# Performance work log

Hardware: AMD Instinct MI355X
Metric: run time of the kernel (lower is better)

## Reference

```python
import jax, jax.numpy as jnp
import numpy as np
import math

EPS = 1e-5

def make_coords(H, W):
    # Faithful port of generate_coordinates (batch-independent; channels 8,9 stay zero).
    cy = H / 2.0 - 0.5
    cx = W / 2.0 - 0.5
    gx, gy = np.meshgrid(np.arange(H, dtype=np.float32), np.arange(W, dtype=np.float32), indexing='ij')
    two_pi = 2.0 * math.pi
    theta = np.arctan2(gy - cx, gx - cy) % two_pi
    theta = np.round(10000.0 * theta) / 10000.0
    coords = np.zeros((H, W, 18), dtype=np.float32)
    adds = [(1, 1), (1, 0), (1, -1), (0, 1), None, (0, -1), (-1, 1), (-1, 0), (-1, -1)]
    for k, add in enumerate(adds):
        if add is None:
            continue  # center tap offset left at zero (as in source)
        n = k if k < 4 else k - 1
        a = theta + n * (two_pi / 8.0)
        coords[:, :, 2 * k] = np.cos(a) + add[0]
        coords[:, :, 2 * k + 1] = np.sin(a) + add[1]
    return jnp.asarray(coords)

def bilinear_sample(x, py, px):
    # x: [B,C,H,W]; py/px: [H,W] sample coords; zero outside boundaries (torchvision semantics).
    H, W = x.shape[2], x.shape[3]
    y0f = jnp.floor(py); x0f = jnp.floor(px)
    wy1 = py - y0f; wy0 = 1.0 - wy1
    wx1 = px - x0f; wx0 = 1.0 - wx1
    def gather(yf, xf):
        valid = ((yf >= 0) & (yf < H) & (xf >= 0) & (xf < W)).astype(x.dtype)
        yi = jnp.clip(yf, 0, H - 1).astype(jnp.int32)
        xi = jnp.clip(xf, 0, W - 1).astype(jnp.int32)
        return x[:, :, yi, xi] * valid  # [B,C,H,W]
    return (gather(y0f, x0f) * (wy0 * wx0) + gather(y0f, x0f + 1) * (wy0 * wx1)
            + gather(y0f + 1, x0f) * (wy1 * wx0) + gather(y0f + 1, x0f + 1) * (wy1 * wx1))

def deform_conv(x, coords, weight, pad=1):
    # x: [B,Cin,H,W]; coords: [H,W,18] with (dy,dx) pairs per 3x3 tap; weight: [Cout,Cin,3,3]; no bias.
    B, C, H, W = x.shape
    ys = jnp.arange(H, dtype=x.dtype)[:, None]
    xs = jnp.arange(W, dtype=x.dtype)[None, :]
    out = jnp.zeros((B, weight.shape[0], H, W), x.dtype)
    for k in range(9):  # fixed 3x3 taps
        kh, kw = k // 3, k % 3
        py = ys - pad + kh + coords[..., 2 * k]
        px = xs - pad + kw + coords[..., 2 * k + 1]
        samp = bilinear_sample(x, py, px)
        out = out + jnp.einsum('bchw,oc->bohw', samp, weight[:, :, kh, kw])
    return out

def bn_relu(x, gamma, beta):
    # BatchNorm2d in training mode (batch statistics, biased variance) + ReLU.
    mu = x.mean(axis=(0, 2, 3), keepdims=True)
    var = ((x - mu) ** 2).mean(axis=(0, 2, 3), keepdims=True)
    xn = (x - mu) * jax.lax.rsqrt(var + EPS)
    return jax.nn.relu(xn * gamma[None, :, None, None] + beta[None, :, None, None])

def maxpool2(x):
    B, C, H, W = x.shape
    return x.reshape(B, C, H // 2, 2, W // 2, 2).max(axis=(3, 5))

def setup_inputs() -> dict:
    key = jax.random.key(0)
    ks = jax.random.split(key, 16)
    B = 1024
    def conv_w(k, co, ci):
        return jax.random.normal(k, (co, ci, 3, 3), jnp.float32) * (1.0 / np.sqrt(ci * 9))
    inp = {
        'x': jax.random.normal(ks[0], (B, 1, 32, 32), jnp.float32),
        'w11': conv_w(ks[1], 32, 1),  'g11': jnp.ones(32),  'b11': jnp.zeros(32),
        'w12': conv_w(ks[2], 32, 32), 'g12': jnp.ones(32),  'b12': jnp.zeros(32),
        'w21': conv_w(ks[3], 64, 32), 'g21': jnp.ones(64),  'b21': jnp.zeros(64),
        'w22': conv_w(ks[4], 64, 64), 'g22': jnp.ones(64),  'b22': jnp.zeros(64),
        'w31': conv_w(ks[5], 128, 64),  'g31': jnp.ones(128), 'b31': jnp.zeros(128),
        'w32': conv_w(ks[6], 128, 128), 'g32': jnp.ones(128), 'b32': jnp.zeros(128),
        'fcw': jax.random.normal(ks[7], (10, 128), jnp.float32) * (1.0 / np.sqrt(128)),
        'fcb': jnp.zeros(10),
        'c32': make_coords(32, 32),
        'c16': make_coords(16, 16),
        'c8': make_coords(8, 8),
    }
    return inp

def reference(x, w11, g11, b11, w12, g12, b12, w21, g21, b21, w22, g22, b22,
              w31, g31, b31, w32, g32, b32, fcw, fcb, c32, c16, c8):
    x = bn_relu(deform_conv(x, c32, w11), g11, b11)
    x = bn_relu(deform_conv(x, c32, w12), g12, b12)
    x = maxpool2(x)                      # [B,32,16,16]
    x = bn_relu(deform_conv(x, c16, w21), g21, b21)
    x = bn_relu(deform_conv(x, c16, w22), g22, b22)
    x = maxpool2(x)                      # [B,64,8,8]
    x = bn_relu(deform_conv(x, c8, w31), g31, b31)
    x = bn_relu(deform_conv(x, c8, w32), g32, b32)
    x = x.mean(axis=(2, 3))              # AvgPool2d(8) over full 8x8 -> [B,128]
    return x @ fcw.T + fcb               # [B,10]
```

## Files before the change

kernel.cpp:

```cpp
#include <hip/hip_runtime.h>
#include <math.h>


#define BATCH 1024
typedef unsigned short u16;
typedef unsigned int uint;
typedef _Float16 f16;
typedef __attribute__((ext_vector_type(2))) _Float16 f16x2;
typedef __attribute__((ext_vector_type(8))) _Float16 f16x8;
typedef __attribute__((ext_vector_type(4))) float f32x4;

__device__ __forceinline__ float b2f(u16 v) {
    return __uint_as_float(((uint)v) << 16);
}
__device__ __forceinline__ float ldf(const void* p, long long i, int isbf) {
    return isbf ? b2f(((const u16*)p)[i]) : ((const float*)p)[i];
}
__device__ __forceinline__ f16x2 u2h2(uint u) {
    union { uint u; f16x2 h; } c; c.u = u; return c.h;
}
__device__ __forceinline__ uint h22u(f16x2 h) {
    union { uint u; f16x2 h; } c; c.h = h; return c.u;
}
__device__ __forceinline__ float h2f(u16 v) {
    union { u16 u; f16 h; } c; c.u = v; return (float)c.h;
}
__device__ __forceinline__ u16 f2h(float f) {
    union { u16 u; f16 h; } c; c.h = (f16)f; return c.u;
}
__device__ __forceinline__ f16x2 pkh(float a, float b) {
    union { decltype(__builtin_amdgcn_cvt_pkrtz(0.f, 0.f)) v; f16x2 h; } c;
    c.v = __builtin_amdgcn_cvt_pkrtz(a, b);
    return c.h;
}

struct Ptrs { const void* p[24]; int sz[24]; };

__global__ __launch_bounds__(256) void probe_dtype(Ptrs P, int* __restrict__ flags)
{
    int t = blockIdx.x;
    bool ones = (t == 2 || t == 5 || t == 8 || t == 11 || t == 14 || t == 17);
    bool inh  = (t == 3 || t == 6 || t == 9 || t == 12 || t == 15 || t == 18 || t == 20);
    if (inh) return;
    const u16* q = (const u16*)P.p[t];
    if (ones) {
        if (threadIdx.x == 0) {
            uint w0 = *(const uint*)q;
            flags[t] = (w0 == 0x3F803F80u) ? 1 : 0;
        }
        return;
    }
    int n = P.sz[t]; if (n > 4096) n = 4096;
    __shared__ int cnt;
    if (threadIdx.x == 0) cnt = 0;
    __syncthreads();
    int local = 0;
    for (int i = threadIdx.x; i < n; i += 256) {
        uint e = (q[i] >> 7) & 0xFFu;
        if (!(e == 0u || (e >= 100u && e <= 140u))) local++;
    }
    atomicAdd(&cnt, local);
    __syncthreads();
    if (threadIdx.x == 0) flags[t] = (cnt * 8 > n) ? 0 : 1;
}

__global__ void fixup_flags(int* __restrict__ flags)
{
    if (threadIdx.x == 0) {
        flags[3] = flags[2];  flags[6] = flags[5];  flags[9] = flags[8];
        flags[12] = flags[11]; flags[15] = flags[14]; flags[18] = flags[17];
        flags[20] = flags[19];
    }
}

__device__ void table_body(const void* coords, int H, int W,
                           int* tIdx, float* tW, int fcd, int i)
{
    int HW = H * W;
    if (i >= HW * 9) return;
    int p = i / 9, k = i % 9;
    int h = p / W, w = p % W;
    int kh = k / 3, kw = k % 3;
    float py = (float)(h - 1 + kh) + ldf(coords, p * 18 + 2 * k, fcd);
    float px = (float)(w - 1 + kw) + ldf(coords, p * 18 + 2 * k + 1, fcd);
    float y0f = floorf(py), x0f = floorf(px);
    float wy1 = py - y0f, wy0 = 1.0f - wy1;
    float wx1 = px - x0f, wx0 = 1.0f - wx1;
    int y0 = (int)y0f, x0 = (int)x0f;
#pragma unroll
    for (int j = 0; j < 4; ++j) {
        int dy = j >> 1, dx = j & 1;
        int yy = y0 + dy, xx = x0 + dx;
        bool valid = (yy >= 0) && (yy < H) && (xx >= 0) && (xx < W);
        int yc = min(max(yy, 0), H - 1);
        int xc = min(max(xx, 0), W - 1);
        tIdx[i * 4 + j] = yc * W + xc;
        tW[i * 4 + j] = valid ? (dy ? wy1 : wy0) * (dx ? wx1 : wx0) : 0.0f;
    }
}

__global__ __launch_bounds__(256) void build_tables(
    const void* c32, const void* c16, const void* c8,
    int* tI32, float* tW32, int* tI16, float* tW16, int* tI8, float* tW8,
    const int* __restrict__ flags)
{
    int b = blockIdx.x, t = threadIdx.x;
    if (b < 36)      table_body(c32, 32, 32, tI32, tW32, flags[21], b * 256 + t);
    else if (b < 45) table_body(c16, 16, 16, tI16, tW16, flags[22], (b - 36) * 256 + t);
    else             table_body(c8, 8, 8, tI8, tW8, flags[23], (b - 45) * 256 + t);
}

__global__ __launch_bounds__(256) void transpose_in(
    const void* __restrict__ x, u16* __restrict__ X0, const int* __restrict__ flags)
{
    int fx = flags[0];
    int p = blockIdx.x;
    int t = threadIdx.x;
    ushort4 v;
    v.x = f2h(ldf(x, (long long)(4 * t + 0) * 1024 + p, fx));
    v.y = f2h(ldf(x, (long long)(4 * t + 1) * 1024 + p, fx));
    v.z = f2h(ldf(x, (long long)(4 * t + 2) * 1024 + p, fx));
    v.w = f2h(ldf(x, (long long)(4 * t + 3) * 1024 + p, fx));
    ((ushort4*)(X0 + (size_t)p * BATCH))[t] = v;
}

__device__ void wb_body(const void* W, u16* Wb, int Cout, int Cin, int fw, int i)
{
    int c8 = i & 7;
    int r = i >> 3;
    int m = r % Cout;
    int r2 = r / Cout;
    int noct = Cin >> 3;
    int oc = r2 % noct;
    int k = r2 / noct;
    int c = oc * 8 + c8;
    Wb[i] = f2h(ldf(W, (long long)m * Cin * 9 + c * 9 + k, fw));
}

__global__ __launch_bounds__(256) void prep_all(
    const void* w11, const void* w12, const void* w21, const void* w22,
    const void* w31, const void* w32,
    float* w11p, u16* wb12, u16* wb21, u16* wb22, u16* wb31, u16* wb32,
    const int* __restrict__ flags)
{
    int i = blockIdx.x * 256 + threadIdx.x;
    if (i < 288) {
        int o = i / 9, k = i % 9;
        w11p[k * 32 + o] = ldf(w11, i, flags[1]);
    } else if (i < 9504)   wb_body(w12, wb12, 32, 32, flags[4], i - 288);
    else if (i < 27936)    wb_body(w21, wb21, 64, 32, flags[7], i - 9504);
    else if (i < 64800)    wb_body(w22, wb22, 64, 64, flags[10], i - 27936);
    else if (i < 138528)   wb_body(w31, wb31, 128, 64, flags[13], i - 64800);
    else if (i < 285984)   wb_body(w32, wb32, 128, 128, flags[16], i - 138528);
}

__global__ __launch_bounds__(256) void conv_l11(
    const u16* __restrict__ X0, const float* __restrict__ W2,
    u16* __restrict__ Y, const int* __restrict__ tIdx, const float* __restrict__ tW)
{
    const int id = blockIdx.x;
    const int p = id >> 1;
    const int oBase = (id & 1) * 16;
    const int b4 = threadIdx.x;
    const ushort4* Xu = (const ushort4*)X0;

    float4 acc[16];
#pragma unroll
    for (int o = 0; o < 16; ++o) acc[o] = make_float4(0.f, 0.f, 0.f, 0.f);

#pragma unroll
    for (int k = 0; k < 9; ++k) {
        float4 s = make_float4(0.f, 0.f, 0.f, 0.f);
#pragma unroll
        for (int j = 0; j < 4; ++j) {
            float wgt = tW[p * 36 + k * 4 + j];
            int pix = tIdx[p * 36 + k * 4 + j];
            ushort4 vv = Xu[pix * 256 + b4];
            s.x = fmaf(wgt, h2f(vv.x), s.x); s.y = fmaf(wgt, h2f(vv.y), s.y);
            s.z = fmaf(wgt, h2f(vv.z), s.z); s.w = fmaf(wgt, h2f(vv.w), s.w);
        }
#pragma unroll
        for (int o = 0; o < 16; ++o) {
            float wv = W2[k * 32 + oBase + o];
            acc[o].x = fmaf(wv, s.x, acc[o].x); acc[o].y = fmaf(wv, s.y, acc[o].y);
            acc[o].z = fmaf(wv, s.z, acc[o].z); acc[o].w = fmaf(wv, s.w, acc[o].w);
        }
    }
#pragma unroll
    for (int bb = 0; bb < 4; ++bb) {
        u16 h[16];
#pragma unroll
        for (int o = 0; o < 16; ++o) h[o] = f2h((&acc[o].x)[bb]);
        uint4 pk;
        pk.x = (uint)h[0] | ((uint)h[1] << 16);
        pk.y = (uint)h[2] | ((uint)h[3] << 16);
        pk.z = (uint)h[4] | ((uint)h[5] << 16);
        pk.w = (uint)h[6] | ((uint)h[7] << 16);
        uint4 pk2;
        pk2.x = (uint)h[8] | ((uint)h[9] << 16);
        pk2.y = (uint)h[10] | ((uint)h[11] << 16);
        pk2.z = (uint)h[12] | ((uint)h[13] << 16);
        pk2.w = (uint)h[14] | ((uint)h[15] << 16);
        size_t base = ((size_t)p * 1024 + 4 * b4 + bb) * 32 + oBase;
        *(uint4*)(Y + base) = pk;
        *(uint4*)(Y + base + 8) = pk2;
    }
}

template<int MF, int NF, int BNORM>
__global__ __launch_bounds__(256) void conv_mfma(
    const u16* __restrict__ X, const u16* __restrict__ Wb,
    u16* __restrict__ Y,
    const int* __restrict__ tIdx, const float* __restrict__ tW,
    int Cin, int Cout, int HW, int pshift,
    const float* __restrict__ stats, const void* __restrict__ gamma,
    const void* __restrict__ beta, const int* __restrict__ flags,
    int gslot, int bslot, float invN)
{
    __shared__ float sSC[128], sSH[128];
    if (BNORM) {
        if (threadIdx.x < Cin) {
            int c = threadIdx.x;
            float mean = stats[2 * c] * invN;
            float var = stats[2 * c + 1] * invN - mean * mean;
            float sc = ldf(gamma, c, flags[gslot]) * rsqrtf(var + 1e-5f);
            sSC[c] = sc;
            sSH[c] = ldf(beta, c, flags[bslot]) - mean * sc;
        }
        __syncthreads();
    }

    const int tid = threadIdx.x;
    const int wid = tid >> 6;
    const int lane = tid & 63;
    const int quad = lane >> 4;
    const int l16 = lane & 15;

    const int pper = HW >> 3;
    const int xcd = blockIdx.x & 7;
    const int lid = blockIdx.x >> 3;
    const int p = xcd * pper + (lid & (pper - 1));
    const int yq = lid >> pshift;

    const int nb = yq * (4 * NF * 16);
    const int wn = wid * (NF * 16);

    const int noct = Cin >> 3;
    const size_t pixstride = (size_t)1024 * Cin;

    int roff[NF];
#pragma unroll
    for (int nf = 0; nf < NF; ++nf)
        roff[nf] = (nb + wn + nf * 16 + l16) * Cin + quad * 8;

    f32x4 acc[MF][NF];
#pragma unroll
    for (int mf = 0; mf < MF; ++mf)
#pragma unroll
        for (int nf = 0; nf < NF; ++nf)
            acc[mf][nf] = (f32x4){0.f, 0.f, 0.f, 0.f};

    const f16x2 zeroh = (f16x2){(f16)0, (f16)0};
    const int nc = Cin >> 5;
    for (int cc = 0; cc < nc; ++cc) {
        const int coff = cc << 5;
        f16x2 sc2[4], sh2[4];
        if (BNORM) {
            int c0 = coff + quad * 8;
#pragma unroll
            for (int i = 0; i < 4; ++i) {
                sc2[i] = pkh(sSC[c0 + 2 * i], sSC[c0 + 2 * i + 1]);
                sh2[i] = pkh(sSH[c0 + 2 * i], sSH[c0 + 2 * i + 1]);
            }
        }
        for (int k = 0; k < 9; ++k) {
            int pix[4]; f16x2 wwh[4];
#pragma unroll
            for (int j = 0; j < 4; ++j) {
                pix[j] = __builtin_amdgcn_readfirstlane(tIdx[p * 36 + k * 4 + j]);
                float w = __uint_as_float(__builtin_amdgcn_readfirstlane(
                    __float_as_uint(tW[p * 36 + k * 4 + j])));
                wwh[j] = pkh(w, w);
            }
            const u16* xb0 = X + (size_t)pix[0] * pixstride;
            const u16* xb1 = X + (size_t)pix[1] * pixstride;
            const u16* xb2 = X + (size_t)pix[2] * pixstride;
            const u16* xb3 = X + (size_t)pix[3] * pixstride;

            f16x8 bf[NF];
#pragma unroll
            for (int nf = 0; nf < NF; ++nf) {
                int ro = roff[nf] + coff;
                uint4 v0 = *(const uint4*)(xb0 + ro);
                uint4 v1 = *(const uint4*)(xb1 + ro);
                uint4 v2 = *(const uint4*)(xb2 + ro);
                uint4 v3 = *(const uint4*)(xb3 + ro);
                const uint* a0 = &v0.x; const uint* a1 = &v1.x;
                const uint* a2 = &v2.x; const uint* a3 = &v3.x;
                union { f16x8 h; uint4 u; } cvt;
                uint o[4];
#pragma unroll
                for (int i = 0; i < 4; ++i) {
                    f16x2 t0 = u2h2(a0[i]), t1 = u2h2(a1[i]);
                    f16x2 t2 = u2h2(a2[i]), t3 = u2h2(a3[i]);
                    if (BNORM) {
                        t0 = __builtin_elementwise_max(t0 * sc2[i] + sh2[i], zeroh);
                        t1 = __builtin_elementwise_max(t1 * sc2[i] + sh2[i], zeroh);
                        t2 = __builtin_elementwise_max(t2 * sc2[i] + sh2[i], zeroh);
                        t3 = __builtin_elementwise_max(t3 * sc2[i] + sh2[i], zeroh);
                    }
                    f16x2 a = t0 * wwh[0];
                    a = t1 * wwh[1] + a;
                    a = t2 * wwh[2] + a;
                    a = t3 * wwh[3] + a;
                    o[i] = h22u(a);
                }
                cvt.u.x = o[0]; cvt.u.y = o[1]; cvt.u.z = o[2]; cvt.u.w = o[3];
                bf[nf] = cvt.h;
            }
            const u16* wk = Wb + ((size_t)(k * noct + (cc << 2) + quad) * Cout + l16) * 8;
#pragma unroll
            for (int mf = 0; mf < MF; ++mf) {
                const f16x8 af = *(const f16x8*)(wk + (size_t)mf * 16 * 8);
#pragma unroll
                for (int nf = 0; nf < NF; ++nf)
                    acc[mf][nf] = __builtin_amdgcn_mfma_f32_16x16x32_f16(
                        af, bf[nf], acc[mf][nf], 0, 0, 0);
            }
        }
    }

#pragma unroll
    for (int mf = 0; mf < MF; ++mf) {
        int cout0 = mf * 16 + quad * 4;
#pragma unroll
        for (int nf = 0; nf < NF; ++nf) {
            int b = nb + wn + nf * 16 + l16;
            uint2 pk;
            pk.x = h22u(pkh(acc[mf][nf][0], acc[mf][nf][1]));
            pk.y = h22u(pkh(acc[mf][nf][2], acc[mf][nf][3]));
            *(uint2*)(Y + ((size_t)p * 1024 + b) * Cout + cout0) = pk;
        }
    }
}

__global__ __launch_bounds__(256) void bn_stats2(
    const u16* __restrict__ Y, float* __restrict__ stats, int Cin, long long NPB)
{
    const int stride = Cin >> 3;
    const int RPI = 256 / stride;
    const int t = threadIdx.x;
    const int cg = t % stride;
    const int r = t / stride;
    const int lane = t & 63;
    const int wid = t >> 6;

    float s[8], q[8];
#pragma unroll
    for (int j = 0; j < 8; ++j) { s[j] = 0.f; q[j] = 0.f; }

    for (long long row0 = (long long)blockIdx.x * RPI; row0 < NPB;
         row0 += (long long)gridDim.x * RPI) {
        long long row = row0 + r;
        if (row >= NPB) continue;
        uint4 v = *(const uint4*)(Y + row * Cin + cg * 8);
        uint ua[4] = {v.x, v.y, v.z, v.w};
#pragma unroll
        for (int jj = 0; jj < 4; ++jj) {
            f16x2 h = u2h2(ua[jj]);
            float lo = (float)h.x, hi = (float)h.y;
            s[2 * jj] += lo;     q[2 * jj] += lo * lo;
            s[2 * jj + 1] += hi; q[2 * jj + 1] += hi * hi;
        }
    }
    for (int off = 32; off >= stride; off >>= 1) {
#pragma unroll
        for (int j = 0; j < 8; ++j) {
            s[j] += __shfl_down(s[j], off);
            q[j] += __shfl_down(q[j], off);
        }
    }
    __shared__ float rs[4][128], rq[4][128];
    if (lane < stride) {
#pragma unroll
        for (int j = 0; j < 8; ++j) {
            rs[wid][lane * 8 + j] = s[j];
            rq[wid][lane * 8 + j] = q[j];
        }
    }
    __syncthreads();
    if (t < Cin) {
        float S = rs[0][t] + rs[1][t] + rs[2][t] + rs[3][t];
        float Q = rq[0][t] + rq[1][t] + rq[2][t] + rq[3][t];
        atomicAdd(&stats[2 * t], S);
        atomicAdd(&stats[2 * t + 1], Q);
    }
}

__global__ __launch_bounds__(256) void pool_bn(
    const u16* __restrict__ A, u16* __restrict__ P,
    const float* __restrict__ stats,
    const void* __restrict__ gamma, const void* __restrict__ beta,
    const int* __restrict__ flags, int gslot, int bslot,
    int H2, int W2, int C, float invN, long long total)
{
    __shared__ float sSC[128], sSH[128];
    if (threadIdx.x < C) {
        int c = threadIdx.x;
        float mean = stats[2 * c] * invN;
        float var = stats[2 * c + 1] * invN - mean * mean;
        float sc = ldf(gamma, c, flags[gslot]) * rsqrtf(var + 1e-5f);
        sSC[c] = sc;
        sSH[c] = ldf(beta, c, flags[bslot]) - mean * sc;
    }
    __syncthreads();
    long long i = (long long)blockIdx.x * 256 + threadIdx.x;
    if (i >= total) return;
    int cgn = C >> 3;
    int cg = (int)(i % cgn);
    long long row = i / cgn;
    int b = (int)(row & 1023);
    int p2 = (int)(row >> 10);
    int h2 = p2 / W2, w2 = p2 % W2;
    int W = 2 * W2;
    int p00 = (2 * h2) * W + 2 * w2;
    const u16* base = A + (size_t)cg * 8;
    uint4 va = *(const uint4*)(base + ((size_t)(p00)*1024 + b) * C);
    uint4 vb = *(const uint4*)(base + ((size_t)(p00 + 1) * 1024 + b) * C);
    uint4 vd = *(const uint4*)(base + ((size_t)(p00 + W) * 1024 + b) * C);
    uint4 ve = *(const uint4*)(base + ((size_t)(p00 + W + 1) * 1024 + b) * C);
    uint ra[4] = {va.x, va.y, va.z, va.w};
    uint rb[4] = {vb.x, vb.y, vb.z, vb.w};
    uint rd[4] = {vd.x, vd.y, vd.z, vd.w};
    uint re[4] = {ve.x, ve.y, ve.z, ve.w};
    uint ro[4];
#pragma unroll
    for (int j = 0; j < 4; ++j) {
        int c = cg * 8 + 2 * j;
        f16x2 ha = u2h2(ra[j]), hb = u2h2(rb[j]), hd = u2h2(rd[j]), he = u2h2(re[j]);
        f16x2 hm = __builtin_elementwise_max(
            __builtin_elementwise_max(ha, hb), __builtin_elementwise_max(hd, he));
        float lo = fmaxf(fmaf((float)hm.x, sSC[c], sSH[c]), 0.f);
        float hi = fmaxf(fmaf((float)hm.y, sSC[c + 1], sSH[c + 1]), 0.f);
        ro[j] = h22u(pkh(lo, hi));
    }
    uint4 m; m.x = ro[0]; m.y = ro[1]; m.z = ro[2]; m.w = ro[3];
    *(uint4*)(P + ((size_t)p2 * 1024 + b) * C + cg * 8) = m;
}

__global__ __launch_bounds__(256) void avg_bn(
    const u16* __restrict__ A, float* __restrict__ M,
    const float* __restrict__ stats,
    const void* __restrict__ gamma, const void* __restrict__ beta,
    const int* __restrict__ flags, int gslot, int bslot, float invN)
{
    __shared__ float sSC[128], sSH[128];
    if (threadIdx.x < 128) {
        int c = threadIdx.x;
        float mean = stats[2 * c] * invN;
        float var = stats[2 * c + 1] * invN - mean * mean;
        float sc = ldf(gamma, c, flags[gslot]) * rsqrtf(var + 1e-5f);
        sSC[c] = sc;
        sSH[c] = ldf(beta, c, flags[bslot]) - mean * sc;
    }
    __syncthreads();
    int i = blockIdx.x * 256 + threadIdx.x;
    int b = i >> 4, cg = i & 15;
    float s[8];
#pragma unroll
    for (int j = 0; j < 8; ++j) s[j] = 0.f;
    for (int p = 0; p < 64; ++p) {
        uint4 v = *(const uint4*)(A + ((size_t)p * 1024 + b) * 128 + cg * 8);
        uint ua[4] = {v.x, v.y, v.z, v.w};
#pragma unroll
        for (int jj = 0; jj < 4; ++jj) {
            int c = cg * 8 + 2 * jj;
            f16x2 h = u2h2(ua[jj]);
            s[2 * jj] += fmaxf(fmaf((float)h.x, sSC[c], sSH[c]), 0.f);
            s[2 * jj + 1] += fmaxf(fmaf((float)h.y, sSC[c + 1], sSH[c + 1]), 0.f);
        }
    }
#pragma unroll
    for (int j = 0; j < 8; ++j) M[(size_t)b * 128 + cg * 8 + j] = s[j] * (1.0f / 64.0f);
}

__global__ __launch_bounds__(256) void fc_naive(
    const float* __restrict__ M, const void* __restrict__ fcw,
    const void* __restrict__ fcb, float* __restrict__ out, int total,
    const int* __restrict__ flags)
{
    int fw = flags[19], fb = flags[20];
    int i = blockIdx.x * 256 + threadIdx.x;
    if (i >= total) return;
    int o = i % 10, b = i / 10;
    float acc = ldf(fcb, o, fb);
    const float* Mb = M + (size_t)b * 128;
    for (int c = 0; c < 128; ++c) acc = fmaf(Mb[c], ldf(fcw, (size_t)o * 128 + c, fw), acc);
    out[i] = acc;
}

__global__ __launch_bounds__(256) void sentinel_k(float* out, int n, float v) {
    int i = blockIdx.x * 256 + threadIdx.x;
    if (i < n) out[i] = v;
}

extern "C" void kernel_launch(void* const* d_in, const int* in_sizes, int n_in,
                              void* d_out, int out_size, void* d_ws, size_t ws_size,
                              hipStream_t stream) {
    float* out = (float*)d_out;

    static const int exp_sizes[24] = {
        1024 * 1024,
        288, 32, 32,   9216, 32, 32,   18432, 64, 64,   36864, 64, 64,
        73728, 128, 128,   147456, 128, 128,
        1280, 10,   18432, 4608, 1152
    };
    float bad = 0.0f;
    if (n_in != 24) bad = 1000.0f;
    else {
        for (int i = 0; i < 24; ++i)
            if (in_sizes[i] != exp_sizes[i]) { bad = 2000.0f + 16.0f * i; break; }
    }
    if (bad != 0.0f) {
        sentinel_k<<<(out_size + 255) / 256, 256, 0, stream>>>(out, out_size, bad);
        return;
    }

    Ptrs P;
    for (int i = 0; i < 24; ++i) { P.p[i] = d_in[i]; P.sz[i] = in_sizes[i]; }

    char* wsb = (char*)d_ws;
    size_t off = 0;
    auto take = [&](size_t bytes) -> void* {
        void* pp = wsb + off;
        off += (bytes + 255) & ~(size_t)255;
        return pp;
    };
    int*   flags = (int*)  take(32 * 4);
    float* stats = (float*)take(6 * 256 * 4);
    int*   tI32  = (int*)  take(1024 * 36 * 4);
    float* tW32  = (float*)take(1024 * 36 * 4);
    int*   tI16  = (int*)  take(256 * 36 * 4);
    float* tW16  = (float*)take(256 * 36 * 4);
    int*   tI8   = (int*)  take(64 * 36 * 4);
    float* tW8   = (float*)take(64 * 36 * 4);
    float* w11p  = (float*)take(32 * 9 * 4);
    u16*   wb12  = (u16*)  take(32 * 32 * 9 * 2);
    u16*   wb21  = (u16*)  take(64 * 32 * 9 * 2);
    u16*   wb22  = (u16*)  take(64 * 64 * 9 * 2);
    u16*   wb31  = (u16*)  take(128 * 64 * 9 * 2);
    u16*   wb32  = (u16*)  take(128 * 128 * 9 * 2);
    u16*   X0    = (u16*)  take((size_t)1024 * BATCH * 2);
    float* M     = (float*)take((size_t)BATCH * 128 * 4);
    u16*   bufA  = (u16*)  take((size_t)32 * 1024 * BATCH * 2);
    u16*   bufB  = (u16*)  take((size_t)32 * 1024 * BATCH * 2);

    if (ws_size < off) {
        sentinel_k<<<(out_size + 255) / 256, 256, 0, stream>>>(out, out_size, 12345.0f);
        return;
    }

    probe_dtype<<<24, 256, 0, stream>>>(P, flags);
    fixup_flags<<<1, 64, 0, stream>>>(flags);
    hipMemsetAsync(stats, 0, 6 * 256 * 4, stream);
    build_tables<<<48, 256, 0, stream>>>(d_in[21], d_in[22], d_in[23],
                                         tI32, tW32, tI16, tW16, tI8, tW8, flags);
    transpose_in<<<1024, 256, 0, stream>>>(d_in[0], X0, flags);
    prep_all<<<1118, 256, 0, stream>>>(d_in[1], d_in[4], d_in[7], d_in[10], d_in[13], d_in[16],
                                       w11p, wb12, wb21, wb22, wb31, wb32, flags);

    float* st0 = stats + 0 * 256;
    float* st1 = stats + 1 * 256;
    float* st2 = stats + 2 * 256;
    float* st3 = stats + 3 * 256;
    float* st4 = stats + 4 * 256;
    float* st5 = stats + 5 * 256;

    conv_l11<<<2048, 256, 0, stream>>>(X0, w11p, bufA, tI32, tW32);
    bn_stats2<<<256, 256, 0, stream>>>(bufA, st0, 32, 1048576LL);
    conv_mfma<2, 2, 1><<<8192, 256, 0, stream>>>(bufA, wb12, bufB, tI32, tW32, 32, 32, 1024, 7,
                                                 st0, d_in[2], d_in[3], flags, 2, 3, 1.0f / 1048576.0f);
    bn_stats2<<<256, 256, 0, stream>>>(bufB, st1, 32, 1048576LL);
    pool_bn<<<4096, 256, 0, stream>>>(bufB, bufA, st1, d_in[5], d_in[6], flags, 5, 6,
                                      16, 16, 32, 1.0f / 1048576.0f, 1048576LL);
    conv_mfma<4, 2, 0><<<2048, 256, 0, stream>>>(bufA, wb21, bufB, tI16, tW16, 32, 64, 256, 5,
                                                 st0, d_in[2], d_in[3], flags, 2, 3, 0.f);
    bn_stats2<<<256, 256, 0, stream>>>(bufB, st2, 64, 262144LL);
    conv_mfma<4, 2, 1><<<2048, 256, 0, stream>>>(bufB, wb22, bufA, tI16, tW16, 64, 64, 256, 5,
                                                 st2, d_in[8], d_in[9], flags, 8, 9, 1.0f / 262144.0f);
    bn_stats2<<<256, 256, 0, stream>>>(bufA, st3, 64, 262144LL);
    pool_bn<<<2048, 256, 0, stream>>>(bufA, bufB, st3, d_in[11], d_in[12], flags, 11, 12,
                                      8, 8, 64, 1.0f / 262144.0f, 524288LL);
    conv_mfma<8, 1, 0><<<1024, 256, 0, stream>>>(bufB, wb31, bufA, tI8, tW8, 64, 128, 64, 3,
                                                 st0, d_in[2], d_in[3], flags, 2, 3, 0.f);
    bn_stats2<<<256, 256, 0, stream>>>(bufA, st4, 128, 65536LL);
    conv_mfma<8, 1, 1><<<1024, 256, 0, stream>>>(bufA, wb32, bufB, tI8, tW8, 128, 128, 64, 3,
                                                 st4, d_in[14], d_in[15], flags, 14, 15, 1.0f / 65536.0f);
    bn_stats2<<<256, 256, 0, stream>>>(bufB, st5, 128, 65536LL);
    avg_bn<<<64, 256, 0, stream>>>(bufB, M, st5, d_in[17], d_in[18], flags, 17, 18,
                                   1.0f / 65536.0f);
    fc_naive<<<40, 256, 0, stream>>>(M, d_in[19], d_in[20], out, 10240, flags);
}
```

Before: 866.7 us.

## Fuse BatchNorm statistics into conv epilogues with per-block partials and reduction

```diff
diff --git a/kernel.cpp b/kernel.cpp
--- a/kernel.cpp
+++ b/kernel.cpp
@@ -154,9 +154,34 @@
     else if (i < 285984)   wb_body(w32, wb32, 128, 128, flags[16], i - 138528);
 }
 
+__global__ __launch_bounds__(256) void reduce_stats(
+    const float* __restrict__ scratch, float* __restrict__ stats, int C, int nblk)
+{
+    int c = blockIdx.x;
+    float s = 0.f, q = 0.f;
+    for (int b = threadIdx.x; b < nblk; b += 256) {
+        s += scratch[(size_t)b * 2 * C + 2 * c];
+        q += scratch[(size_t)b * 2 * C + 2 * c + 1];
+    }
+#pragma unroll
+    for (int d = 1; d < 64; d <<= 1) {
+        s += __shfl_xor(s, d);
+        q += __shfl_xor(q, d);
+    }
+    __shared__ float ls[4], lq[4];
+    int wid = threadIdx.x >> 6, lane = threadIdx.x & 63;
+    if (lane == 0) { ls[wid] = s; lq[wid] = q; }
+    __syncthreads();
+    if (threadIdx.x == 0) {
+        stats[2 * c] = (ls[0] + ls[1]) + (ls[2] + ls[3]);
+        stats[2 * c + 1] = (lq[0] + lq[1]) + (lq[2] + lq[3]);
+    }
+}
+
 __global__ __launch_bounds__(256) void conv_l11(
     const u16* __restrict__ X0, const float* __restrict__ W2,
-    u16* __restrict__ Y, const int* __restrict__ tIdx, const float* __restrict__ tW)
+    u16* __restrict__ Y, const int* __restrict__ tIdx, const float* __restrict__ tW,
+    float* __restrict__ scratch)
 {
     const int id = blockIdx.x;
     const int p = id >> 1;
@@ -205,6 +230,31 @@
         *(uint4*)(Y + base) = pk;
         *(uint4*)(Y + base + 8) = pk2;
     }
+    __shared__ float rS[4][16], rQ[4][16];
+    int wid = threadIdx.x >> 6, lane = threadIdx.x & 63;
+#pragma unroll
+    for (int o = 0; o < 16; ++o) {
+        float s = (acc[o].x + acc[o].y) + (acc[o].z + acc[o].w);
+        float q = (acc[o].x * acc[o].x + acc[o].y * acc[o].y)
+                + (acc[o].z * acc[o].z + acc[o].w * acc[o].w);
+#pragma unroll
+        for (int d = 1; d < 64; d <<= 1) {
+            s += __shfl_xor(s, d);
+            q += __shfl_xor(q, d);
+        }
+        if (lane == 0) { rS[wid][o] = s; rQ[wid][o] = q; }
+    }
+    __syncthreads();
+    if (threadIdx.x < 64) {
+        int c = threadIdx.x >> 1, isq = threadIdx.x & 1;
+        float v = 0.f;
+        if ((c >> 4) == (id & 1)) {
+            int o = c & 15;
+            v = isq ? (rQ[0][o] + rQ[1][o]) + (rQ[2][o] + rQ[3][o])
+                    : (rS[0][o] + rS[1][o]) + (rS[2][o] + rS[3][o]);
+        }
+        scratch[(size_t)id * 64 + threadIdx.x] = v;
+    }
 }
 
 template<int MF, int NF, int BNORM>
@@ -215,9 +265,10 @@
     int Cin, int Cout, int HW, int pshift,
     const float* __restrict__ stats, const void* __restrict__ gamma,
     const void* __restrict__ beta, const int* __restrict__ flags,
-    int gslot, int bslot, float invN)
+    int gslot, int bslot, float invN, float* __restrict__ scratch)
 {
     __shared__ float sSC[128], sSH[128];
+    __shared__ float rS[4][128], rQ[4][128];
     if (BNORM) {
         if (threadIdx.x < Cin) {
             int c = threadIdx.x;
@@ -342,58 +393,34 @@
             *(uint2*)(Y + ((size_t)p * 1024 + b) * Cout + cout0) = pk;
         }
     }
-}
-
-__global__ __launch_bounds__(256) void bn_stats2(
-    const u16* __restrict__ Y, float* __restrict__ stats, int Cin, long long NPB)
-{
-    const int stride = Cin >> 3;
-    const int RPI = 256 / stride;
-    const int t = threadIdx.x;
-    const int cg = t % stride;
-    const int r = t / stride;
-    const int lane = t & 63;
-    const int wid = t >> 6;
-
-    float s[8], q[8];
-#pragma unroll
-    for (int j = 0; j < 8; ++j) { s[j] = 0.f; q[j] = 0.f; }
-
-    for (long long row0 = (long long)blockIdx.x * RPI; row0 < NPB;
-         row0 += (long long)gridDim.x * RPI) {
-        long long row = row0 + r;
-        if (row >= NPB) continue;
-        uint4 v = *(const uint4*)(Y + row * Cin + cg * 8);
-        uint ua[4] = {v.x, v.y, v.z, v.w};
-#pragma unroll
-        for (int jj = 0; jj < 4; ++jj) {
-            f16x2 h = u2h2(ua[jj]);
-            float lo = (float)h.x, hi = (float)h.y;
-            s[2 * jj] += lo;     q[2 * jj] += lo * lo;
-            s[2 * jj + 1] += hi; q[2 * jj + 1] += hi * hi;
-        }
-    }
-    for (int off = 32; off >= stride; off >>= 1) {
-#pragma unroll
-        for (int j = 0; j < 8; ++j) {
-            s[j] += __shfl_down(s[j], off);
-            q[j] += __shfl_down(q[j], off);
-        }
-    }
-    __shared__ float rs[4][128], rq[4][128];
-    if (lane < stride) {
-#pragma unroll
-        for (int j = 0; j < 8; ++j) {
-            rs[wid][lane * 8 + j] = s[j];
-            rq[wid][lane * 8 + j] = q[j];
-        }
-    }
+
+#pragma unroll
+    for (int mf = 0; mf < MF; ++mf)
+#pragma unroll
+        for (int reg = 0; reg < 4; ++reg) {
+            float s = 0.f, q = 0.f;
+#pragma unroll
+            for (int nf = 0; nf < NF; ++nf) {
+                float v = acc[mf][nf][reg];
+                s += v; q += v * v;
+            }
+#pragma unroll
+            for (int d = 1; d < 16; d <<= 1) {
+                s += __shfl_xor(s, d);
+                q += __shfl_xor(q, d);
+            }
+            if (l16 == 0) {
+                int c = mf * 16 + quad * 4 + reg;
+                rS[wid][c] = s;
+                rQ[wid][c] = q;
+            }
+        }
     __syncthreads();
-    if (t < Cin) {
-        float S = rs[0][t] + rs[1][t] + rs[2][t] + rs[3][t];
-        float Q = rq[0][t] + rq[1][t] + rq[2][t] + rq[3][t];
-        atomicAdd(&stats[2 * t], S);
-        atomicAdd(&stats[2 * t + 1], Q);
+    if (tid < 2 * Cout) {
+        int c = tid >> 1, isq = tid & 1;
+        float v = isq ? (rQ[0][c] + rQ[1][c]) + (rQ[2][c] + rQ[3][c])
+                      : (rS[0][c] + rS[1][c]) + (rS[2][c] + rS[3][c]);
+        scratch[(size_t)blockIdx.x * 2 * Cout + tid] = v;
     }
 }
 
@@ -538,6 +565,7 @@
     };
     int*   flags = (int*)  take(32 * 4);
     float* stats = (float*)take(6 * 256 * 4);
+    float* scr   = (float*)take((size_t)8192 * 64 * 4);
     int*   tI32  = (int*)  take(1024 * 36 * 4);
     float* tW32  = (float*)take(1024 * 36 * 4);
     int*   tI16  = (int*)  take(256 * 36 * 4);
@@ -562,7 +590,6 @@
 
     probe_dtype<<<24, 256, 0, stream>>>(P, flags);
     fixup_flags<<<1, 64, 0, stream>>>(flags);
-    hipMemsetAsync(stats, 0, 6 * 256 * 4, stream);
     build_tables<<<48, 256, 0, stream>>>(d_in[21], d_in[22], d_in[23],
                                          tI32, tW32, tI16, tW16, tI8, tW8, flags);
     transpose_in<<<1024, 256, 0, stream>>>(d_in[0], X0, flags);
@@ -576,27 +603,30 @@
     float* st4 = stats + 4 * 256;
     float* st5 = stats + 5 * 256;
 
-    conv_l11<<<2048, 256, 0, stream>>>(X0, w11p, bufA, tI32, tW32);
-    bn_stats2<<<256, 256, 0, stream>>>(bufA, st0, 32, 1048576LL);
+    conv_l11<<<2048, 256, 0, stream>>>(X0, w11p, bufA, tI32, tW32, scr);
+    reduce_stats<<<32, 256, 0, stream>>>(scr, st0, 32, 2048);
     conv_mfma<2, 2, 1><<<8192, 256, 0, stream>>>(bufA, wb12, bufB, tI32, tW32, 32, 32, 1024, 7,
-                                                 st0, d_in[2], d_in[3], flags, 2, 3, 1.0f / 1048576.0f);
-    bn_stats2<<<256, 256, 0, stream>>>(bufB, st1, 32, 1048576LL);
+                                                 st0, d_in[2], d_in[3], flags, 2, 3,
+                                                 1.0f / 1048576.0f, scr);
+    reduce_stats<<<32, 256, 0, stream>>>(scr, st1, 32, 8192);
     pool_bn<<<4096, 256, 0, stream>>>(bufB, bufA, st1, d_in[5], d_in[6], flags, 5, 6,
                                       16, 16, 32, 1.0f / 1048576.0f, 1048576LL);
     conv_mfma<4, 2, 0><<<2048, 256, 0, stream>>>(bufA, wb21, bufB, tI16, tW16, 32, 64, 256, 5,
-                                                 st0, d_in[2], d_in[3], flags, 2, 3, 0.f);
-    bn_stats2<<<256, 256, 0, stream>>>(bufB, st2, 64, 262144LL);
+                                                 st0, d_in[2], d_in[3], flags, 2, 3, 0.f, scr);
+    reduce_stats<<<64, 256, 0, stream>>>(scr, st2, 64, 2048);
     conv_mfma<4, 2, 1><<<2048, 256, 0, stream>>>(bufB, wb22, bufA, tI16, tW16, 64, 64, 256, 5,
-                                                 st2, d_in[8], d_in[9], flags, 8, 9, 1.0f / 262144.0f);
-    bn_stats2<<<256, 256, 0, stream>>>(bufA, st3, 64, 262144LL);
+                                                 st2, d_in[8], d_in[9], flags, 8, 9,
+                                                 1.0f / 262144.0f, scr);
+    reduce_stats<<<64, 256, 0, stream>>>(scr, st3, 64, 2048);
     pool_bn<<<2048, 256, 0, stream>>>(bufA, bufB, st3, d_in[11], d_in[12], flags, 11, 12,
                                       8, 8, 64, 1.0f / 262144.0f, 524288LL);
     conv_mfma<8, 1, 0><<<1024, 256, 0, stream>>>(bufB, wb31, bufA, tI8, tW8, 64, 128, 64, 3,
-                                                 st0, d_in[2], d_in[3], flags, 2, 3, 0.f);
-    bn_stats2<<<256, 256, 0, stream>>>(bufA, st4, 128, 65536LL);
+                                                 st0, d_in[2], d_in[3], flags, 2, 3, 0.f, scr);
+    reduce_stats<<<128, 256, 0, stream>>>(scr, st4, 128, 1024);
     conv_mfma<8, 1, 1><<<1024, 256, 0, stream>>>(bufA, wb32, bufB, tI8, tW8, 128, 128, 64, 3,
-                                                 st4, d_in[14], d_in[15], flags, 14, 15, 1.0f / 65536.0f);
-    bn_stats2<<<256, 256, 0, stream>>>(bufB, st5, 128, 65536LL);
+                                                 st4, d_in[14], d_in[15], flags, 14, 15,
+                                                 1.0f / 65536.0f, scr);
+    reduce_stats<<<128, 256, 0, stream>>>(scr, st5, 128, 1024);
     avg_bn<<<64, 256, 0, stream>>>(bufB, M, st5, d_in[17], d_in[18], flags, 17, 18,
                                    1.0f / 65536.0f);
     fc_naive<<<40, 256, 0, stream>>>(M, d_in[19], d_in[20], out, 10240, flags);
```

Measured after the change: 775.2 us (median of 2 runs). 1.12x faster.
